# Kernel tuning notes

Measured on AMD Instinct MI355X. Metric: run time of the kernel, lower is better.

Reference implementation:

```python
import jax, jax.numpy as jnp
import numpy as np

N_QUBITS = 10
DEPTH = 5
DIM = 2 ** N_QUBITS  # 1024
NUM_CLASSES = 2
BATCH = 16384
IN_DIM = 784


def _rot_matrices(w):
    # w: [depth, n_qubits, 3] angles (phi, theta, omega); qml.Rot = RZ(omega) RY(theta) RZ(phi)
    phi, theta, omega = w[..., 0], w[..., 1], w[..., 2]
    c, s = jnp.cos(theta / 2), jnp.sin(theta / 2)
    e = lambda a: jnp.exp(1j * a.astype(jnp.complex64))
    m00 = e(-(phi + omega) / 2) * c
    m01 = -e((phi - omega) / 2) * s
    m10 = e(-(phi - omega) / 2) * s
    m11 = e((phi + omega) / 2) * c
    return jnp.stack([jnp.stack([m00, m01], -1), jnp.stack([m10, m11], -1)], -2)  # [D, n, 2, 2]


def _apply_1q(state, U, w):
    # state: [B] + [2]*n ; apply 2x2 U on qubit axis w
    s = jnp.moveaxis(state, w + 1, -1)
    s = s @ U.T
    return jnp.moveaxis(s, -1, w + 1)


def _apply_cnot(state, c, t):
    s = jnp.moveaxis(state, (c + 1, t + 1), (-2, -1))
    s = jnp.concatenate([s[..., 0:1, :], s[..., 1:2, ::-1]], axis=-2)  # flip target where control=1
    return jnp.moveaxis(s, (-2, -1), (c + 1, t + 1))


def _circuit(x, weights):
    B = x.shape[0]
    # AmplitudeEmbedding: pad_with=0, normalize=True
    amp = jnp.pad(x, ((0, 0), (0, DIM - x.shape[1])))
    amp = amp / jnp.linalg.norm(amp, axis=1, keepdims=True)
    state = amp.astype(jnp.complex64).reshape((B,) + (2,) * N_QUBITS)
    U = _rot_matrices(weights)
    for d in range(DEPTH):
        for i in range(N_QUBITS):  # entangling CNOT ring
            state = _apply_cnot(state, i, (i + 1) % N_QUBITS)
        for i in range(N_QUBITS):  # per-qubit Rot
            state = _apply_1q(state, U[d, i], i)
    probs = (state.real ** 2 + state.imag ** 2).reshape(B, DIM)
    # <Z_i> = P(bit_i = 0) - P(bit_i = 1)
    z = []
    for i in range(N_QUBITS):
        p = probs.reshape(B, 2 ** i, 2, -1)
        z.append(p[:, :, 0, :].sum((1, 2)) - p[:, :, 1, :].sum((1, 2)))
    return jnp.stack(z, axis=1)  # [B, n_qubits]


def setup_inputs() -> dict:
    key = jax.random.key(0)
    k1, k2, k3 = jax.random.split(key, 3)
    x = jax.random.normal(k1, (BATCH, IN_DIM), dtype=jnp.float32)
    weights = jax.random.uniform(k2, (DEPTH, N_QUBITS, 3), dtype=jnp.float32) * (2.0 * np.pi)
    y = jax.random.randint(k3, (BATCH,), 0, NUM_CLASSES)
    return {"x": x, "weights": weights, "y": y}


def reference(x, weights, y):
    logits = _circuit(x, weights)[:, :NUM_CLASSES]
    logp = jax.nn.log_softmax(logits, axis=-1)
    loss = -jnp.take_along_axis(logp, y[:, None], axis=1).mean()
    return loss
```

## Files before the change

### kernel.cpp

```cpp
#include <hip/hip_runtime.h>
#include <type_traits>

#define NQ 10
#define N_DEPTH 5
#define DIM 1024
#define BATCH 16384
#define IN_DIM 784
#define NGATES 50
#define KALLOC 832
#define NT 13
#define NSLOT 768
#define NB 12

typedef float f32x2 __attribute__((ext_vector_type(2)));
typedef float f32x4 __attribute__((ext_vector_type(4)));
typedef unsigned u32x4 __attribute__((ext_vector_type(4)));

struct MaskTab {
  unsigned v[NGATES];
  unsigned p[NGATES];
  unsigned vz0, vz1;
};

constexpr MaskTab make_masks() {
  MaskTab t{};
  unsigned v[NQ], p[NQ];
  for (int i = 0; i < NQ; ++i) { v[i] = 1u << (9 - i); p[i] = 1u << (9 - i); }
  for (int d = 0; d < N_DEPTH; ++d) {
    for (int i = 0; i < NQ; ++i) {
      int c = i, tt = (i + 1) % NQ;
      v[tt] ^= v[c];
      p[c]  ^= p[tt];
    }
    for (int i = 0; i < NQ; ++i) {
      t.v[d * NQ + i] = v[i];
      t.p[d * NQ + i] = p[i];
    }
  }
  t.vz0 = v[0];
  t.vz1 = v[1];
  return t;
}

constexpr MaskTab MT = make_masks();
__constant__ MaskTab d_MT = make_masks();

struct PermTab { short slot[DIM]; };
constexpr PermTab make_perm() {
  PermTab t{};
  int a = 0, b = 256, c = 512;
  for (int m = 0; m < DIM; ++m) {
    const int p0 = __builtin_popcount((unsigned)m & MT.vz0) & 1;
    const int p1 = __builtin_popcount((unsigned)m & MT.vz1) & 1;
    if (p0 && !p1)      t.slot[m] = (short)a++;
    else if (!p0 && p1) t.slot[m] = (short)b++;
    else if (p0 && p1)  t.slot[m] = (short)c++;
    else                t.slot[m] = -1;
  }
  return t;
}
__constant__ PermTab d_PT = make_perm();

__device__ __forceinline__ f32x2 ampfma(f32x2 o, f32x2 q, f32x2 co, f32x2 cp) {
  f32x2 d;
  asm("v_pk_mul_f32 %0, %2, %1 op_sel:[0,0] op_sel_hi:[0,1]\n\t"
      "v_pk_fma_f32 %0, %2, %1, %0 op_sel:[1,1,0] op_sel_hi:[1,0,1] neg_lo:[1,0,0]\n\t"
      "v_pk_fma_f32 %0, %3, %4, %0 op_sel:[0,0,0] op_sel_hi:[0,1,1]\n\t"
      "v_pk_fma_f32 %0, %3, %4, %0 op_sel:[1,1,0] op_sel_hi:[1,0,1] neg_lo:[1,0,0]"
      : "=&v"(d)
      : "v"(o), "v"(co), "v"(cp), "v"(q));
  return d;
}

__device__ __forceinline__ float fxor(float x, unsigned m) {
  return __uint_as_float(__float_as_uint(x) ^ m);
}

__device__ __forceinline__ unsigned pk4_fp8(float a, float b, float c, float d) {
  int v = __builtin_amdgcn_cvt_pk_fp8_f32(a, b, 0, false);
  v = __builtin_amdgcn_cvt_pk_fp8_f32(c, d, v, true);
  return (unsigned)v;
}

__device__ __forceinline__ void gll16(const void* g, void* l) {
  __builtin_amdgcn_global_load_lds(
      (const __attribute__((address_space(1))) void*)g,
      (__attribute__((address_space(3))) void*)l, 16, 0, 0);
}

#define XSCALE 32.0f
#define WSCALE 16.0f
#define SINV   (1.0f / 262144.0f)

__global__ __launch_bounds__(256) void prep(const float* __restrict__ X,
                                            char* __restrict__ Xf8,
                                            float* __restrict__ xn2,
                                            const float* __restrict__ w,
                                            char* __restrict__ W2T) {
  __shared__ f32x4 UL4[NGATES];
  __shared__ f32x2 S0[DIM];
  __shared__ f32x2 S1[DIM];

  const int tid = threadIdx.x;

  if (blockIdx.x >= 832) {
    const int row = (blockIdx.x - 832) * 8 + (tid >> 5);
    const int l32 = tid & 31;
    const float* src = X + (size_t)row * IN_DIM;
    char* dst = Xf8 + (size_t)row * KALLOC;
    float ssq = 0.0f;
    for (int c = l32; c < 52; c += 32) {
      u32x4 out;
      if (c < 49) {
        f32x4 v0 = *(const f32x4*)(src + c * 16);
        f32x4 v1 = *(const f32x4*)(src + c * 16 + 4);
        f32x4 v2 = *(const f32x4*)(src + c * 16 + 8);
        f32x4 v3 = *(const f32x4*)(src + c * 16 + 12);
        ssq += v0.x * v0.x + v0.y * v0.y + v0.z * v0.z + v0.w * v0.w +
               v1.x * v1.x + v1.y * v1.y + v1.z * v1.z + v1.w * v1.w +
               v2.x * v2.x + v2.y * v2.y + v2.z * v2.z + v2.w * v2.w +
               v3.x * v3.x + v3.y * v3.y + v3.z * v3.z + v3.w * v3.w;
        out = u32x4{
          pk4_fp8(v0.x * XSCALE, v0.y * XSCALE, v0.z * XSCALE, v0.w * XSCALE),
          pk4_fp8(v1.x * XSCALE, v1.y * XSCALE, v1.z * XSCALE, v1.w * XSCALE),
          pk4_fp8(v2.x * XSCALE, v2.y * XSCALE, v2.z * XSCALE, v2.w * XSCALE),
          pk4_fp8(v3.x * XSCALE, v3.y * XSCALE, v3.z * XSCALE, v3.w * XSCALE)};
      } else {
        out = u32x4{0, 0, 0, 0};
      }
      *(u32x4*)(dst + c * 16) = out;
    }
#pragma unroll
    for (int off = 1; off < 32; off <<= 1) ssq += __shfl_xor(ssq, off);
    if (l32 == 0) xn2[row] = ssq;
    return;
  }

  if (tid < NGATES) {
    float phi = w[tid * 3 + 0], th = w[tid * 3 + 1], om = w[tid * 3 + 2];
    float ct = cosf(th * 0.5f), st = sinf(th * 0.5f);
    float aa = (phi + om) * 0.5f, bb = (phi - om) * 0.5f;
    float cA = cosf(aa), sA = sinf(aa), cB = cosf(bb), sB = sinf(bb);
    UL4[tid] = f32x4{ ct * cA, -ct * sA, -st * cB, -st * sB };
  }

  const int j = blockIdx.x;

  if (j >= IN_DIM) {
#pragma unroll
    for (int k = 0; k < 3; ++k) {
      const int s = tid + k * 256;
      W2T[(size_t)(2 * s) * KALLOC + j] = 0;
      W2T[(size_t)(2 * s + 1) * KALLOC + j] = 0;
    }
    return;
  }

#pragma unroll
  for (int k = 0; k < 4; ++k) {
    const int m = tid + k * 256;
    S0[m] = f32x2{(m == j) ? 1.0f : 0.0f, 0.0f};
  }
  __syncthreads();

  for (int g = 0; g < NGATES; ++g) {
    const f32x2* src = (g & 1) ? S1 : S0;
    f32x2* dst = (g & 1) ? S0 : S1;
    const f32x4 A = UL4[g];
    const unsigned v = d_MT.v[g];
    const unsigned p = d_MT.p[g];
#pragma unroll
    for (int k = 0; k < 4; ++k) {
      const int m = tid + k * 256;
      f32x2 o = src[m];
      f32x2 q = src[m ^ (int)p];
      const unsigned sg = (unsigned)(__popc((int)((unsigned)m & v)) & 1) << 31;
      const f32x2 co = {A.x, fxor(A.y, sg)};
      const f32x2 cp = {fxor(A.z, sg), A.w};
      dst[m] = ampfma(o, q, co, cp);
    }
    __syncthreads();
  }

  const f32x2* fin = S0;
#pragma unroll
  for (int k = 0; k < 4; ++k) {
    const int m = tid + k * 256;
    const int s = d_PT.slot[m];
    f32x2 a = fin[m];
    if (s >= 0) {
      const unsigned pk = pk4_fp8(a.x * WSCALE, a.y * WSCALE, 0.0f, 0.0f);
      W2T[(size_t)(2 * s) * KALLOC + j] = (char)(pk & 0xffu);
      W2T[(size_t)(2 * s + 1) * KALLOC + j] = (char)((pk >> 8) & 0xffu);
    }
  }
}

__global__ __launch_bounds__(512) void gemm_fused(const char* __restrict__ Xf8,
                                                  const char* __restrict__ W2T,
                                                  float* __restrict__ accb) {
  __shared__ u32x4 lds4[3072];
  char* lds = (char*)lds4;

  const int tid = threadIdx.x;
  const int orig = blockIdx.x;
  const int bx = (orig & 7) * 96 + (orig >> 3);
  const int mb = bx / NB, nb = bx % NB;
  const int m0 = mb * 256, n0 = nb * 128;
  const int lane = tid & 63, wv = tid >> 6;
  const int wm = wv >> 2, wn = wv & 3;

  const int rl = lane >> 2;
  const int csrc = (lane & 3) ^ (rl & 3) ^ ((rl >> 2) & 3);

  auto stage = [&](int t) {
    char* Ab = lds + (t & 1) * 24576;
    char* Bb = Ab + 16384;
    const int col = t * 64 + csrc * 16;
#pragma unroll
    for (int i = 0; i < 2; ++i) {
      const int g = wv * 2 + i;
      const int row = g * 16 + rl;
      gll16(Xf8 + (size_t)(m0 + row) * KALLOC + col, Ab + g * 1024);
    }
    {
      const int row = wv * 16 + rl;
      gll16(W2T + (size_t)(n0 + row) * KALLOC + col, Bb + wv * 1024);
    }
  };

  stage(0);
  asm volatile("s_waitcnt vmcnt(0)" ::: "memory");
  __builtin_amdgcn_s_barrier();

  f32x4 acc[8][2];
#pragma unroll
  for (int fm = 0; fm < 8; ++fm)
#pragma unroll
    for (int fn = 0; fn < 2; ++fn) acc[fm][fn] = f32x4{0, 0, 0, 0};

  const int kc = lane >> 4;

  for (int t = 0; t < NT; ++t) {
    const char* Ab = lds + (t & 1) * 24576;
    const char* Bb = Ab + 16384;

    long af0[8], bf0[2], af1[8], bf1[2];
#pragma unroll
    for (int f = 0; f < 8; ++f) {
      const int ar = wm * 128 + f * 16 + (lane & 15);
      const int sw = (ar & 3) ^ ((ar >> 2) & 3);
      af0[f] = *(const long*)(Ab + ar * 64 + (((kc >> 1) ^ sw) * 16) + (kc & 1) * 8);
    }
#pragma unroll
    for (int f = 0; f < 2; ++f) {
      const int br = wn * 32 + f * 16 + (lane & 15);
      const int sw = (br & 3) ^ ((br >> 2) & 3);
      bf0[f] = *(const long*)(Bb + br * 64 + (((kc >> 1) ^ sw) * 16) + (kc & 1) * 8);
    }
    if (t < NT - 1) stage(t + 1);
#pragma unroll
    for (int f = 0; f < 8; ++f) {
      const int ar = wm * 128 + f * 16 + (lane & 15);
      const int sw = (ar & 3) ^ ((ar >> 2) & 3);
      const int kb = 4 + kc;
      af1[f] = *(const long*)(Ab + ar * 64 + (((kb >> 1) ^ sw) * 16) + (kb & 1) * 8);
    }
#pragma unroll
    for (int f = 0; f < 2; ++f) {
      const int br = wn * 32 + f * 16 + (lane & 15);
      const int sw = (br & 3) ^ ((br >> 2) & 3);
      const int kb = 4 + kc;
      bf1[f] = *(const long*)(Bb + br * 64 + (((kb >> 1) ^ sw) * 16) + (kb & 1) * 8);
    }

    __builtin_amdgcn_s_setprio(1);
#pragma unroll
    for (int fm = 0; fm < 8; ++fm)
#pragma unroll
      for (int fn = 0; fn < 2; ++fn)
        acc[fm][fn] = __builtin_amdgcn_mfma_f32_16x16x32_fp8_fp8(
            af0[fm], bf0[fn], acc[fm][fn], 0, 0, 0);
    __builtin_amdgcn_s_setprio(0);

    __builtin_amdgcn_s_setprio(1);
#pragma unroll
    for (int fm = 0; fm < 8; ++fm)
#pragma unroll
      for (int fn = 0; fn < 2; ++fn)
        acc[fm][fn] = __builtin_amdgcn_mfma_f32_16x16x32_fp8_fp8(
            af1[fm], bf1[fn], acc[fm][fn], 0, 0, 0);
    __builtin_amdgcn_s_setprio(0);

    if (t < NT - 1) {
      asm volatile("s_waitcnt vmcnt(0)" ::: "memory");
      __builtin_amdgcn_sched_barrier(0);
      __builtin_amdgcn_s_barrier();
    }
  }

#pragma unroll
  for (int fm = 0; fm < 8; ++fm) {
    float sn[4] = {0, 0, 0, 0};
#pragma unroll
    for (int fn = 0; fn < 2; ++fn) {
#pragma unroll
      for (int r = 0; r < 4; ++r) {
        const float vv = acc[fm][fn][r];
        sn[r] = fmaf(vv, vv, sn[r]);
      }
    }
#pragma unroll
    for (int off = 1; off < 16; off <<= 1) {
#pragma unroll
      for (int r = 0; r < 4; ++r) sn[r] += __shfl_xor(sn[r], off);
    }
    if ((lane & 15) == 0) {
#pragma unroll
      for (int r = 0; r < 4; ++r) {
        const int m = m0 + wm * 128 + fm * 16 + (lane >> 4) * 4 + r;
        accb[(size_t)nb * BATCH + m] = sn[r];
      }
    }
  }
}

__global__ __launch_bounds__(256) void loss_partial(const float* __restrict__ accb,
                                                    const float* __restrict__ xn2,
                                                    const int* __restrict__ y,
                                                    float* __restrict__ partial) {
  const int s = blockIdx.x * 256 + threadIdx.x;
  float SA = 0.0f, SB = 0.0f, SC = 0.0f;
#pragma unroll
  for (int k = 0; k < 4; ++k) {
    SA += accb[(size_t)(0 + k) * BATCH + s];
    SB += accb[(size_t)(4 + k) * BATCH + s];
    SC += accb[(size_t)(8 + k) * BATCH + s];
  }
  SA *= SINV; SB *= SINV; SC *= SINV;
  const float n2 = xn2[s];
  const float z0 = n2 - 2.0f * (SA + SC);
  const float z1 = n2 - 2.0f * (SB + SC);
  const float inv = 1.0f / n2;
  const float l0 = z0 * inv, l1 = z1 * inv;
  const float mx = fmaxf(l0, l1);
  const float lse = mx + logf(expf(l0 - mx) + expf(l1 - mx));
  float loss = lse - ((y[s] == 0) ? l0 : l1);

  __shared__ float sm[256];
  sm[threadIdx.x] = loss;
  __syncthreads();
  for (int st = 128; st > 0; st >>= 1) {
    if (threadIdx.x < st) sm[threadIdx.x] += sm[threadIdx.x + st];
    __syncthreads();
  }
  if (threadIdx.x == 0) partial[blockIdx.x] = sm[0];
}

__global__ __launch_bounds__(64) void loss_final(const float* __restrict__ partial,
                                                 float* __restrict__ out) {
  float v = partial[threadIdx.x];
#pragma unroll
  for (int off = 1; off < 64; off <<= 1) v += __shfl_xor(v, off);
  if (threadIdx.x == 0) out[0] = v * (1.0f / (float)BATCH);
}

extern "C" void kernel_launch(void* const* d_in, const int* in_sizes, int n_in,
                              void* d_out, int out_size, void* d_ws, size_t ws_size,
                              hipStream_t stream) {
  const float* x = (const float*)d_in[0];
  const float* w = (const float*)d_in[1];
  const int*   y = (const int*)d_in[2];

  char* ws = (char*)d_ws;
  char*     Xf8  = ws;
  char*     W2Tu = ws + 13631488;
  float*    xn2  = (float*)(ws + 14909440);
  float*    accb = (float*)(ws + 14975232);
  float* partial = (float*)(ws + 15761408);

  prep<<<2880, 256, 0, stream>>>(x, Xf8, xn2, w, W2Tu);
  gemm_fused<<<768, 512, 0, stream>>>(Xf8, W2Tu, accb);
  loss_partial<<<BATCH / 256, 256, 0, stream>>>(accb, xn2, y, partial);
  loss_final<<<1, 64, 0, stream>>>(partial, (float*)d_out);
}
```

Baseline: 79.10 us.

## Permute K layout so each lane fetches both MFMA k-halves in one 16-byte LDS read

Reorders the K dimension in both the fp8 X buffer and the W2T matrix so that, within each 64-byte row, a lane's two 8-byte fragments (k-halves 0 and 1) sit next to each other. The GEMM inner loop then issues a single 128-bit LDS load per fragment instead of two 64-bit loads, which halves the LDS instruction count. The trade-off is that both operand fragments are now loaded before staging the next tile, so the first MFMA batch no longer overlaps with the second set of loads. Register pressure may also change.

Result: slower. 81.51 us (+3.0%).

```diff
diff --git a/kernel.cpp b/kernel.cpp
--- a/kernel.cpp
+++ b/kernel.cpp
@@ -15,6 +15,7 @@
 typedef float f32x2 __attribute__((ext_vector_type(2)));
 typedef float f32x4 __attribute__((ext_vector_type(4)));
 typedef unsigned u32x4 __attribute__((ext_vector_type(4)));
+typedef long lx2 __attribute__((ext_vector_type(2)));
 
 struct MaskTab {
   unsigned v[NGATES];
@@ -92,6 +93,7 @@
 #define WSCALE 16.0f
 #define SINV   (1.0f / 262144.0f)
 
+
 __global__ __launch_bounds__(256) void prep(const float* __restrict__ X,
                                             char* __restrict__ Xf8,
                                             float* __restrict__ xn2,
@@ -109,26 +111,28 @@
     const float* src = X + (size_t)row * IN_DIM;
     char* dst = Xf8 + (size_t)row * KALLOC;
     float ssq = 0.0f;
-    for (int c = l32; c < 52; c += 32) {
-      u32x4 out;
-      if (c < 49) {
-        f32x4 v0 = *(const f32x4*)(src + c * 16);
-        f32x4 v1 = *(const f32x4*)(src + c * 16 + 4);
-        f32x4 v2 = *(const f32x4*)(src + c * 16 + 8);
-        f32x4 v3 = *(const f32x4*)(src + c * 16 + 12);
+    for (int b = l32; b < 52; b += 32) {
+      const int g = b >> 2, wq = b & 3;
+      const int k1 = g * 64 + wq * 8;
+      const int k2 = k1 + 32;
+      u32x4 out = u32x4{0, 0, 0, 0};
+      if (k1 < IN_DIM) {
+        f32x4 v0 = *(const f32x4*)(src + k1);
+        f32x4 v1 = *(const f32x4*)(src + k1 + 4);
         ssq += v0.x * v0.x + v0.y * v0.y + v0.z * v0.z + v0.w * v0.w +
-               v1.x * v1.x + v1.y * v1.y + v1.z * v1.z + v1.w * v1.w +
-               v2.x * v2.x + v2.y * v2.y + v2.z * v2.z + v2.w * v2.w +
+               v1.x * v1.x + v1.y * v1.y + v1.z * v1.z + v1.w * v1.w;
+        out.x = pk4_fp8(v0.x * XSCALE, v0.y * XSCALE, v0.z * XSCALE, v0.w * XSCALE);
+        out.y = pk4_fp8(v1.x * XSCALE, v1.y * XSCALE, v1.z * XSCALE, v1.w * XSCALE);
+      }
+      if (k2 < IN_DIM) {
+        f32x4 v2 = *(const f32x4*)(src + k2);
+        f32x4 v3 = *(const f32x4*)(src + k2 + 4);
+        ssq += v2.x * v2.x + v2.y * v2.y + v2.z * v2.z + v2.w * v2.w +
                v3.x * v3.x + v3.y * v3.y + v3.z * v3.z + v3.w * v3.w;
-        out = u32x4{
-          pk4_fp8(v0.x * XSCALE, v0.y * XSCALE, v0.z * XSCALE, v0.w * XSCALE),
-          pk4_fp8(v1.x * XSCALE, v1.y * XSCALE, v1.z * XSCALE, v1.w * XSCALE),
-          pk4_fp8(v2.x * XSCALE, v2.y * XSCALE, v2.z * XSCALE, v2.w * XSCALE),
-          pk4_fp8(v3.x * XSCALE, v3.y * XSCALE, v3.z * XSCALE, v3.w * XSCALE)};
-      } else {
-        out = u32x4{0, 0, 0, 0};
+        out.z = pk4_fp8(v2.x * XSCALE, v2.y * XSCALE, v2.z * XSCALE, v2.w * XSCALE);
+        out.w = pk4_fp8(v3.x * XSCALE, v3.y * XSCALE, v3.z * XSCALE, v3.w * XSCALE);
       }
-      *(u32x4*)(dst + c * 16) = out;
+      *(u32x4*)(dst + b * 16) = out;
     }
 #pragma unroll
     for (int off = 1; off < 32; off <<= 1) ssq += __shfl_xor(ssq, off);
@@ -145,13 +149,15 @@
   }
 
   const int j = blockIdx.x;
+  const int jp = (j >> 6) * 64 + (((j >> 3) & 3) << 4) + (((j >> 5) & 1) << 3)
+                 + (j & 7);
 
   if (j >= IN_DIM) {
 #pragma unroll
     for (int k = 0; k < 3; ++k) {
       const int s = tid + k * 256;
-      W2T[(size_t)(2 * s) * KALLOC + j] = 0;
-      W2T[(size_t)(2 * s + 1) * KALLOC + j] = 0;
+      W2T[(size_t)(2 * s) * KALLOC + jp] = 0;
+      W2T[(size_t)(2 * s + 1) * KALLOC + jp] = 0;
     }
     return;
   }
@@ -190,8 +196,8 @@
     f32x2 a = fin[m];
     if (s >= 0) {
       const unsigned pk = pk4_fp8(a.x * WSCALE, a.y * WSCALE, 0.0f, 0.0f);
-      W2T[(size_t)(2 * s) * KALLOC + j] = (char)(pk & 0xffu);
-      W2T[(size_t)(2 * s + 1) * KALLOC + j] = (char)((pk >> 8) & 0xffu);
+      W2T[(size_t)(2 * s) * KALLOC + jp] = (char)(pk & 0xffu);
+      W2T[(size_t)(2 * s + 1) * KALLOC + jp] = (char)((pk >> 8) & 0xffu);
     }
   }
 }
@@ -250,29 +256,19 @@
     for (int f = 0; f < 8; ++f) {
       const int ar = wm * 128 + f * 16 + (lane & 15);
       const int sw = (ar & 3) ^ ((ar >> 2) & 3);
-      af0[f] = *(const long*)(Ab + ar * 64 + (((kc >> 1) ^ sw) * 16) + (kc & 1) * 8);
+      lx2 va = *(const lx2*)(Ab + ar * 64 + ((kc ^ sw) * 16));
+      af0[f] = va.x;
+      af1[f] = va.y;
     }
 #pragma unroll
     for (int f = 0; f < 2; ++f) {
       const int br = wn * 32 + f * 16 + (lane & 15);
       const int sw = (br & 3) ^ ((br >> 2) & 3);
-      bf0[f] = *(const long*)(Bb + br * 64 + (((kc >> 1) ^ sw) * 16) + (kc & 1) * 8);
+      lx2 vb = *(const lx2*)(Bb + br * 64 + ((kc ^ sw) * 16));
+      bf0[f] = vb.x;
+      bf1[f] = vb.y;
     }
     if (t < NT - 1) stage(t + 1);
-#pragma unroll
-    for (int f = 0; f < 8; ++f) {
-      const int ar = wm * 128 + f * 16 + (lane & 15);
-      const int sw = (ar & 3) ^ ((ar >> 2) & 3);
-      const int kb = 4 + kc;
-      af1[f] = *(const long*)(Ab + ar * 64 + (((kb >> 1) ^ sw) * 16) + (kb & 1) * 8);
-    }
-#pragma unroll
-    for (int f = 0; f < 2; ++f) {
-      const int br = wn * 32 + f * 16 + (lane & 15);
-      const int sw = (br & 3) ^ ((br >> 2) & 3);
-      const int kb = 4 + kc;
-      bf1[f] = *(const long*)(Bb + br * 64 + (((kb >> 1) ^ sw) * 16) + (kb & 1) * 8);
-    }
 
     __builtin_amdgcn_s_setprio(1);
 #pragma unroll
```
